# Kernel optimization log

Hardware: AMD Instinct MI355X
Metric: run time of the kernel (lower is better)

## Reference

```python
import jax, jax.numpy as jnp
import numpy as np

N = 50000      # nodes
E = 600000     # edges (before self-loops)
D_IN = 128     # input feature dim
HID = 128      # hidden_channels
HEADS1 = 8
OUT1 = HID // HEADS1  # 16 per head, concat -> 128
NEG_SLOPE = 0.2       # PyG GATConv default leaky_relu slope


def setup_inputs() -> dict:
    key = jax.random.key(0)
    ks = jax.random.split(key, 12)
    glorot = lambda k, shape: jax.random.normal(k, shape, jnp.float32) * np.sqrt(2.0 / (shape[0] + shape[-1]))
    x = jax.random.normal(ks[0], (N, D_IN), jnp.float32)
    edge_index = jax.random.randint(ks[1], (2, E), 0, N, dtype=jnp.int64)
    W1 = glorot(ks[2], (D_IN, HEADS1 * OUT1))
    att_src1 = glorot(ks[3], (HEADS1, OUT1))
    att_dst1 = glorot(ks[4], (HEADS1, OUT1))
    b1 = jnp.zeros((HEADS1 * OUT1,), jnp.float32)
    W2 = glorot(ks[5], (HID, HID))
    att_src2 = glorot(ks[6], (1, HID))
    att_dst2 = glorot(ks[7], (1, HID))
    b2 = jnp.zeros((HID,), jnp.float32)
    return {"x": x, "edge_index": edge_index,
            "W1": W1, "att_src1": att_src1, "att_dst1": att_dst1, "b1": b1,
            "W2": W2, "att_src2": att_src2, "att_dst2": att_dst2, "b2": b2}


def gat_conv(x, edge_index, W, a_src, a_dst, bias, concat):
    """PyG-style GATConv (eval mode: attention dropout disabled)."""
    n = x.shape[0]
    heads, out_ch = a_src.shape
    # add self-loops (PyG default add_self_loops=True)
    loop = jnp.arange(n, dtype=edge_index.dtype)
    src = jnp.concatenate([edge_index[0], loop])  # message source
    dst = jnp.concatenate([edge_index[1], loop])  # aggregation target
    h = (x @ W).reshape(n, heads, out_ch)                    # [n, H, C]
    alpha_src = jnp.sum(h * a_src[None], axis=-1)            # [n, H]
    alpha_dst = jnp.sum(h * a_dst[None], axis=-1)            # [n, H]
    e = alpha_src[src] + alpha_dst[dst]                      # [E+n, H]
    e = jnp.where(e > 0, e, NEG_SLOPE * e)                   # leaky_relu
    # segment softmax over incoming edges of each destination node
    e_max = jax.ops.segment_max(e, dst, num_segments=n)      # [n, H]
    ex = jnp.exp(e - e_max[dst])
    denom = jax.ops.segment_sum(ex, dst, num_segments=n)     # [n, H]
    alpha = ex / denom[dst]                                  # [E+n, H]
    msg = h[src] * alpha[:, :, None]                         # [E+n, H, C]
    out = jax.ops.segment_sum(msg, dst, num_segments=n)      # [n, H, C]
    out = out.reshape(n, heads * out_ch) if concat else out.mean(axis=1)
    return out + bias


def reference(x, edge_index, W1, att_src1, att_dst1, b1, W2, att_src2, att_dst2, b2):
    # eval mode: F.dropout is identity
    h = jax.nn.elu(gat_conv(x, edge_index, W1, att_src1, att_dst1, b1, concat=True))
    out = gat_conv(h, edge_index, W2, att_src2, att_dst2, b2, concat=False)
    return out
```

## Files before the change

### kernel.cpp

```cpp
#include <hip/hip_runtime.h>
#include <hip/hip_bf16.h>

#define NEG_SLOPE 0.2f

typedef short s16x8 __attribute__((ext_vector_type(8)));
typedef float f32x4 __attribute__((ext_vector_type(4)));

__device__ __forceinline__ unsigned short f2bf(float f) {
    unsigned int u = __float_as_uint(f);
    u += 0x7FFFu + ((u >> 16) & 1u);
    return (unsigned short)(u >> 16);
}


__global__ void zero_kernel(int* __restrict__ p, int count) {
    int i = blockIdx.x * blockDim.x + threadIdx.x;
    if (i < count) p[i] = 0;
}

__global__ __launch_bounds__(256) void hist_kernel(const int* __restrict__ ei, int e, int n,
                                                   int* __restrict__ ghist) {
    __shared__ int lh[256];
    int t = threadIdx.x;
    lh[t] = 0;
    __syncthreads();
    int base = blockIdx.x * 2048;
    int en = e + n;
#pragma unroll
    for (int q = 0; q < 8; ++q) {
        int i = base + q * 256 + t;
        if (i < en) {
            int dst = (i < e) ? ei[e + i] : (i - e);
            atomicAdd(&lh[dst >> 8], 1);
        }
    }
    __syncthreads();
    if (lh[t]) atomicAdd(&ghist[t], lh[t]);
}

__global__ __launch_bounds__(256) void bscan_kernel(const int* __restrict__ ghist,
                                                    int* __restrict__ gbase,
                                                    int* __restrict__ gcursor) {
    __shared__ int s[256];
    int t = threadIdx.x;
    int v = ghist[t];
    s[t] = v;
    __syncthreads();
    for (int off = 1; off < 256; off <<= 1) {
        int u = (t >= off) ? s[t - off] : 0;
        __syncthreads();
        s[t] += u;
        __syncthreads();
    }
    int ex = s[t] - v;
    gbase[t] = ex;
    gcursor[t] = ex;
}

__global__ __launch_bounds__(256) void scatter_kernel(const int* __restrict__ ei, int e, int n,
                                                      int* __restrict__ gcursor,
                                                      unsigned int* __restrict__ gpair) {
    __shared__ int lh[256], lbase[256];
    int t = threadIdx.x;
    lh[t] = 0;
    __syncthreads();
    int base = blockIdx.x * 2048;
    int en = e + n;
    int bk[8], rk[8];
    unsigned int pk[8];
#pragma unroll
    for (int q = 0; q < 8; ++q) {
        int i = base + q * 256 + t;
        bk[q] = -1;
        if (i < en) {
            int src, dst;
            if (i < e) { src = ei[i]; dst = ei[e + i]; }
            else       { src = i - e; dst = i - e; }
            int b = dst >> 8;
            bk[q] = b;
            rk[q] = atomicAdd(&lh[b], 1);
            pk[q] = (unsigned int)src | ((unsigned int)(dst & 255) << 16);
        }
    }
    __syncthreads();
    if (lh[t]) lbase[t] = atomicAdd(&gcursor[t], lh[t]);
    __syncthreads();
#pragma unroll
    for (int q = 0; q < 8; ++q)
        if (bk[q] >= 0) gpair[lbase[bk[q]] + rk[q]] = pk[q];
}

__global__ __launch_bounds__(256) void bucket_csr_kernel(const unsigned int* __restrict__ gpair,
                                                         const int* __restrict__ gbase,
                                                         int* __restrict__ rowptr,
                                                         int* __restrict__ colsrc, int n, int en) {
    int b = blockIdx.x, t = threadIdx.x;
    __shared__ int cnt[256], scn[256], cur[256];
    cnt[t] = 0;
    __syncthreads();
    int beg = gbase[b];
    int end = (b < 255) ? gbase[b + 1] : en;
    for (int i = beg + t; i < end; i += 256)
        atomicAdd(&cnt[gpair[i] >> 16], 1);
    __syncthreads();
    int v = cnt[t];
    scn[t] = v;
    __syncthreads();
    for (int off = 1; off < 256; off <<= 1) {
        int u = (t >= off) ? scn[t - off] : 0;
        __syncthreads();
        scn[t] += u;
        __syncthreads();
    }
    int ex = scn[t] - v;
    cur[t] = ex;
    int node = b * 256 + t;
    if (node < n) rowptr[node] = beg + ex;
    if (b == 0 && t == 0) rowptr[n] = en;
    __syncthreads();
    for (int i = beg + t; i < end; i += 256) {
        unsigned int p = gpair[i];
        int ofs = atomicAdd(&cur[p >> 16], 1);
        colsrc[beg + ofs] = (int)(p & 0xFFFFu);
    }
}


__global__ __launch_bounds__(256) void prep_w_kernel(const float* __restrict__ W1,
                                                     const float* __restrict__ as1,
                                                     const float* __restrict__ ad1,
                                                     unsigned short* __restrict__ Wf1,
                                                     const float* __restrict__ W2,
                                                     const float* __restrict__ as2,
                                                     const float* __restrict__ ad2,
                                                     unsigned short* __restrict__ Wf2) {
    int layer = blockIdx.x >> 2;
    int kt = blockIdx.x & 3;
    const float* W = layer ? W2 : W1;
    const float* as_v = layer ? as2 : as1;
    const float* ad_v = layer ? ad2 : ad1;
    unsigned short* Wf = layer ? Wf2 : Wf1;
    int H = layer ? 1 : 8;
    int t = threadIdx.x;
    for (int task = t; task < 9 * 64; task += 256) {
        int ct = task / 64, l = task & 63;
        int kbase = kt * 32 + (l >> 4) * 8;
        int c = l & 15;
        unsigned short o[8];
        if (ct < 8) {
            int col = ct * 16 + c;
#pragma unroll
            for (int j = 0; j < 8; ++j) o[j] = f2bf(W[(size_t)(kbase + j) * 128 + col]);
        } else {
#pragma unroll
            for (int j = 0; j < 8; ++j) {
                float s = 0.f;
                if (H == 8) {
                    const float* a = (c < 8) ? as_v : ad_v;
                    int hh = c & 7;
                    for (int m = 0; m < 16; ++m)
                        s += W[(size_t)(kbase + j) * 128 + hh * 16 + m] * a[hh * 16 + m];
                } else if (c < 2) {
                    const float* a = (c == 0) ? as_v : ad_v;
                    for (int m = 0; m < 128; ++m)
                        s += W[(size_t)(kbase + j) * 128 + m] * a[m];
                }
                o[j] = f2bf(s);
            }
        }
        *(uint4*)&Wf[(((size_t)kt * 9 + ct) * 64 + l) * 8] = *(uint4*)o;
    }
}


template <int H, bool INBF16>
__global__ __launch_bounds__(256) void gemm_mfma_kernel(const void* __restrict__ Xv,
                                                        const unsigned short* __restrict__ Wf,
                                                        unsigned short* __restrict__ Ob,
                                                        float* __restrict__ as_out,
                                                        float* __restrict__ ad_out, int n) {
    __shared__ unsigned short lds[26624];
    int tid = threadIdx.x;
    int row0 = blockIdx.x * 64;

    {
        const uint4* src = (const uint4*)Wf;
        uint4* dst = (uint4*)&lds[8192];
#pragma unroll
        for (int i = 0; i < 9; ++i) dst[tid + 256 * i] = src[tid + 256 * i];
    }
#pragma unroll
    for (int q = 0; q < 4; ++q) {
        int task = tid + q * 256;
        int r = task >> 4, kc = task & 15;
        int gr = row0 + r;
        uint4 val = make_uint4(0, 0, 0, 0);
        if (gr < n) {
            if (INBF16) {
                val = *(const uint4*)((const unsigned short*)Xv + (size_t)gr * 128 + kc * 8);
            } else {
                const float4* xp = (const float4*)((const float*)Xv + (size_t)gr * 128 + kc * 8);
                float4 x0 = xp[0], x1 = xp[1];
                unsigned short o[8] = {f2bf(x0.x), f2bf(x0.y), f2bf(x0.z), f2bf(x0.w),
                                       f2bf(x1.x), f2bf(x1.y), f2bf(x1.z), f2bf(x1.w)};
                val = *(uint4*)o;
            }
        }
        int w = r >> 4, kt = kc >> 2, lane = ((kc & 3) << 4) + (r & 15);
        *(uint4*)&lds[(size_t)(((w * 4 + kt) * 64) + lane) * 8] = val;
    }
    __syncthreads();

    int w = tid >> 6, l = tid & 63;
    f32x4 acc[9];
#pragma unroll
    for (int ct = 0; ct < 9; ++ct) acc[ct] = (f32x4){0.f, 0.f, 0.f, 0.f};
#pragma unroll
    for (int kt = 0; kt < 4; ++kt) {
        s16x8 a = *(s16x8*)&lds[(size_t)((w * 4 + kt) * 64 + l) * 8];
#pragma unroll
        for (int ct = 0; ct < 9; ++ct) {
            s16x8 b = *(s16x8*)&lds[8192 + (size_t)((kt * 9 + ct) * 64 + l) * 8];
            acc[ct] = __builtin_amdgcn_mfma_f32_16x16x32_bf16(a, b, acc[ct], 0, 0, 0);
        }
    }

    int c = l & 15, rgrp = l >> 4;
    int rowb = row0 + w * 16 + rgrp * 4;
#pragma unroll
    for (int reg = 0; reg < 4; ++reg) {
        int row = rowb + reg;
        if (row < n) {
#pragma unroll
            for (int ct = 0; ct < 8; ++ct)
                Ob[(size_t)row * 128 + ct * 16 + c] = f2bf(acc[ct][reg]);
            float av = acc[8][reg];
            if (H == 8) {
                if (c < 8) as_out[(size_t)row * 8 + c] = av;
                else       ad_out[(size_t)row * 8 + (c - 8)] = av;
            } else {
                if (c == 0)      as_out[row] = av;
                else if (c == 1) ad_out[row] = av;
            }
        }
    }
}


template <int H, int OBF>
__global__ __launch_bounds__(256) void agg_kernel(const int* __restrict__ rowptr,
                                                  const int* __restrict__ colsrc,
                                                  const unsigned short* __restrict__ hb,
                                                  const float* __restrict__ as,
                                                  const float* __restrict__ ad,
                                                  const float* __restrict__ bias,
                                                  void* __restrict__ outv, int n) {
    int tid = threadIdx.x;
    int node = blockIdx.x * 8 + (tid >> 5);
    int sub = tid & 31;
    int slot = sub >> 4;
    int cl = sub & 15;
    if (node >= n) return;
    int beg = rowptr[node];
    int end = rowptr[node + 1];
    int head = (H == 8) ? (cl >> 1) : 0;
    float adh = ad[(size_t)node * H + head];

    float acc[8];
#pragma unroll
    for (int c = 0; c < 8; ++c) acc[c] = 0.f;
    float den = 0.f;

#pragma unroll 2
    for (int i = beg + slot; i < end; i += 2) {
        int s = colsrc[i];
        float ev = as[(size_t)s * H + head] + adh;
        ev = (ev > 0.f) ? ev : NEG_SLOPE * ev;
        float wgt = __expf(ev);
        den += wgt;
        uint4 a = *(const uint4*)(hb + (size_t)s * 128 + cl * 8);
        unsigned int u[4] = {a.x, a.y, a.z, a.w};
#pragma unroll
        for (int k = 0; k < 4; ++k) {
            float lo = __uint_as_float(u[k] << 16);
            float hi = __uint_as_float(u[k] & 0xffff0000u);
            acc[2 * k]     += wgt * lo;
            acc[2 * k + 1] += wgt * hi;
        }
    }

    den += __shfl_xor(den, 16, 64);
#pragma unroll
    for (int c = 0; c < 8; ++c) acc[c] += __shfl_xor(acc[c], 16, 64);

    if (slot == 0) {
        float inv = 1.0f / den;
        float r[8];
#pragma unroll
        for (int k = 0; k < 8; ++k) {
            r[k] = acc[k] * inv + bias[cl * 8 + k];
            if (OBF) r[k] = (r[k] > 0.f) ? r[k] : expm1f(r[k]);
        }
        if (OBF) {
            unsigned short o[8];
#pragma unroll
            for (int k = 0; k < 8; ++k) o[k] = f2bf(r[k]);
            *(uint4*)((unsigned short*)outv + (size_t)node * 128 + cl * 8) = *(uint4*)o;
        } else {
            float4* p = (float4*)((float*)outv + (size_t)node * 128 + cl * 8);
            p[0] = make_float4(r[0], r[1], r[2], r[3]);
            p[1] = make_float4(r[4], r[5], r[6], r[7]);
        }
    }
}


extern "C" void kernel_launch(void* const* d_in, const int* in_sizes, int n_in,
                              void* d_out, int out_size, void* d_ws, size_t ws_size,
                              hipStream_t stream) {
    const float* x    = (const float*)d_in[0];
    const int*   ei   = (const int*)d_in[1];
    const float* W1   = (const float*)d_in[2];
    const float* a_s1 = (const float*)d_in[3];
    const float* a_d1 = (const float*)d_in[4];
    const float* b1   = (const float*)d_in[5];
    const float* W2   = (const float*)d_in[6];
    const float* a_s2 = (const float*)d_in[7];
    const float* a_d2 = (const float*)d_in[8];
    const float* b2   = (const float*)d_in[9];

    const int n  = in_sizes[0] / 128;
    const int e  = in_sizes[1] / 2;
    const int en = e + n;
    const int nbuck = (n + 255) >> 8;
    const int echunks = (en + 2047) / 2048;

    char* ws = (char*)d_ws;
    size_t off = 0;
    auto alloc = [&](size_t bytes) -> void* {
        void* p = ws + off;
        off += (bytes + 255) & ~(size_t)255;
        return p;
    };
    unsigned short* hb   = (unsigned short*)alloc((size_t)n * 128 * 2);
    unsigned short* hmid = (unsigned short*)alloc((size_t)n * 128 * 2);
    float* as1    = (float*)alloc((size_t)n * 8 * 4);
    float* ad1    = (float*)alloc((size_t)n * 8 * 4);
    float* as2    = (float*)alloc((size_t)n * 4);
    float* ad2    = (float*)alloc((size_t)n * 4);
    int*   rowptr = (int*)alloc((size_t)(n + 1) * 4);
    int*   colsrc = (int*)alloc((size_t)en * 4);
    unsigned int* gpair = (unsigned int*)alloc((size_t)en * 4);
    int*   ghist  = (int*)alloc(256 * 4);
    int*   gbase  = (int*)alloc(256 * 4);
    int*   gcursor= (int*)alloc(256 * 4);
    unsigned short* Wf1 = (unsigned short*)alloc(4 * 9 * 64 * 8 * 2);
    unsigned short* Wf2 = (unsigned short*)alloc(4 * 9 * 64 * 8 * 2);

    zero_kernel<<<1, 256, 0, stream>>>(ghist, 256);
    hist_kernel<<<echunks, 256, 0, stream>>>(ei, e, n, ghist);
    bscan_kernel<<<1, 256, 0, stream>>>(ghist, gbase, gcursor);
    scatter_kernel<<<echunks, 256, 0, stream>>>(ei, e, n, gcursor, gpair);
    bucket_csr_kernel<<<nbuck, 256, 0, stream>>>(gpair, gbase, rowptr, colsrc, n, en);

    prep_w_kernel<<<8, 256, 0, stream>>>(W1, a_s1, a_d1, Wf1, W2, a_s2, a_d2, Wf2);

    int gemm_grid = (n + 63) / 64;
    int node_grid = (n + 7) / 8;

    gemm_mfma_kernel<8, false><<<gemm_grid, 256, 0, stream>>>(x, Wf1, hb, as1, ad1, n);
    agg_kernel<8, 1><<<node_grid, 256, 0, stream>>>(rowptr, colsrc, hb, as1, ad1, b1, hmid, n);

    gemm_mfma_kernel<1, true><<<gemm_grid, 256, 0, stream>>>(hmid, Wf2, hb, as2, ad2, n);
    agg_kernel<1, 0><<<node_grid, 256, 0, stream>>>(rowptr, colsrc, hb, as2, ad2, b2, d_out, n);

    (void)n_in; (void)out_size; (void)ws_size;
}
```

Measured before the change: 149.4 us.

## Drop histogram pass with fixed-capacity buckets and read GEMM weights from global

After: 133.6 us. -10.5%, faster.

```diff
diff --git a/kernel.cpp b/kernel.cpp
--- a/kernel.cpp
+++ b/kernel.cpp
@@ -2,6 +2,7 @@
 #include <hip/hip_bf16.h>
 
 #define NEG_SLOPE 0.2f
+#define BCAP 8192
 
 typedef short s16x8 __attribute__((ext_vector_type(8)));
 typedef float f32x4 __attribute__((ext_vector_type(4)));
@@ -10,119 +11,6 @@
     unsigned int u = __float_as_uint(f);
     u += 0x7FFFu + ((u >> 16) & 1u);
     return (unsigned short)(u >> 16);
-}
-
-
-__global__ void zero_kernel(int* __restrict__ p, int count) {
-    int i = blockIdx.x * blockDim.x + threadIdx.x;
-    if (i < count) p[i] = 0;
-}
-
-__global__ __launch_bounds__(256) void hist_kernel(const int* __restrict__ ei, int e, int n,
-                                                   int* __restrict__ ghist) {
-    __shared__ int lh[256];
-    int t = threadIdx.x;
-    lh[t] = 0;
-    __syncthreads();
-    int base = blockIdx.x * 2048;
-    int en = e + n;
-#pragma unroll
-    for (int q = 0; q < 8; ++q) {
-        int i = base + q * 256 + t;
-        if (i < en) {
-            int dst = (i < e) ? ei[e + i] : (i - e);
-            atomicAdd(&lh[dst >> 8], 1);
-        }
-    }
-    __syncthreads();
-    if (lh[t]) atomicAdd(&ghist[t], lh[t]);
-}
-
-__global__ __launch_bounds__(256) void bscan_kernel(const int* __restrict__ ghist,
-                                                    int* __restrict__ gbase,
-                                                    int* __restrict__ gcursor) {
-    __shared__ int s[256];
-    int t = threadIdx.x;
-    int v = ghist[t];
-    s[t] = v;
-    __syncthreads();
-    for (int off = 1; off < 256; off <<= 1) {
-        int u = (t >= off) ? s[t - off] : 0;
-        __syncthreads();
-        s[t] += u;
-        __syncthreads();
-    }
-    int ex = s[t] - v;
-    gbase[t] = ex;
-    gcursor[t] = ex;
-}
-
-__global__ __launch_bounds__(256) void scatter_kernel(const int* __restrict__ ei, int e, int n,
-                                                      int* __restrict__ gcursor,
-                                                      unsigned int* __restrict__ gpair) {
-    __shared__ int lh[256], lbase[256];
-    int t = threadIdx.x;
-    lh[t] = 0;
-    __syncthreads();
-    int base = blockIdx.x * 2048;
-    int en = e + n;
-    int bk[8], rk[8];
-    unsigned int pk[8];
-#pragma unroll
-    for (int q = 0; q < 8; ++q) {
-        int i = base + q * 256 + t;
-        bk[q] = -1;
-        if (i < en) {
-            int src, dst;
-            if (i < e) { src = ei[i]; dst = ei[e + i]; }
-            else       { src = i - e; dst = i - e; }
-            int b = dst >> 8;
-            bk[q] = b;
-            rk[q] = atomicAdd(&lh[b], 1);
-            pk[q] = (unsigned int)src | ((unsigned int)(dst & 255) << 16);
-        }
-    }
-    __syncthreads();
-    if (lh[t]) lbase[t] = atomicAdd(&gcursor[t], lh[t]);
-    __syncthreads();
-#pragma unroll
-    for (int q = 0; q < 8; ++q)
-        if (bk[q] >= 0) gpair[lbase[bk[q]] + rk[q]] = pk[q];
-}
-
-__global__ __launch_bounds__(256) void bucket_csr_kernel(const unsigned int* __restrict__ gpair,
-                                                         const int* __restrict__ gbase,
-                                                         int* __restrict__ rowptr,
-                                                         int* __restrict__ colsrc, int n, int en) {
-    int b = blockIdx.x, t = threadIdx.x;
-    __shared__ int cnt[256], scn[256], cur[256];
-    cnt[t] = 0;
-    __syncthreads();
-    int beg = gbase[b];
-    int end = (b < 255) ? gbase[b + 1] : en;
-    for (int i = beg + t; i < end; i += 256)
-        atomicAdd(&cnt[gpair[i] >> 16], 1);
-    __syncthreads();
-    int v = cnt[t];
-    scn[t] = v;
-    __syncthreads();
-    for (int off = 1; off < 256; off <<= 1) {
-        int u = (t >= off) ? scn[t - off] : 0;
-        __syncthreads();
-        scn[t] += u;
-        __syncthreads();
-    }
-    int ex = scn[t] - v;
-    cur[t] = ex;
-    int node = b * 256 + t;
-    if (node < n) rowptr[node] = beg + ex;
-    if (b == 0 && t == 0) rowptr[n] = en;
-    __syncthreads();
-    for (int i = beg + t; i < end; i += 256) {
-        unsigned int p = gpair[i];
-        int ofs = atomicAdd(&cur[p >> 16], 1);
-        colsrc[beg + ofs] = (int)(p & 0xFFFFu);
-    }
 }
 
 
@@ -133,15 +21,23 @@
                                                      const float* __restrict__ W2,
                                                      const float* __restrict__ as2,
                                                      const float* __restrict__ ad2,
-                                                     unsigned short* __restrict__ Wf2) {
-    int layer = blockIdx.x >> 2;
-    int kt = blockIdx.x & 3;
+                                                     unsigned short* __restrict__ Wf2,
+                                                     int* __restrict__ gcursor,
+                                                     int* __restrict__ rowptr, int n, int en) {
+    int bid = blockIdx.x;
+    int t = threadIdx.x;
+    if (bid == 8) {
+        gcursor[t] = 0;
+        if (t == 0) rowptr[n] = en;
+        return;
+    }
+    int layer = bid >> 2;
+    int kt = bid & 3;
     const float* W = layer ? W2 : W1;
     const float* as_v = layer ? as2 : as1;
     const float* ad_v = layer ? ad2 : ad1;
     unsigned short* Wf = layer ? Wf2 : Wf1;
     int H = layer ? 1 : 8;
-    int t = threadIdx.x;
     for (int task = t; task < 9 * 64; task += 256) {
         int ct = task / 64, l = task & 63;
         int kbase = kt * 32 + (l >> 4) * 8;
@@ -173,22 +69,94 @@
 }
 
 
+__global__ __launch_bounds__(256) void scatter_kernel(const int* __restrict__ ei, int e, int n,
+                                                      int* __restrict__ gcursor,
+                                                      unsigned int* __restrict__ gpair) {
+    __shared__ int lh[256], lbase[256];
+    int t = threadIdx.x;
+    lh[t] = 0;
+    __syncthreads();
+    int base = blockIdx.x * 2048;
+    int en = e + n;
+    int bk[8], rk[8];
+    unsigned int pk[8];
+#pragma unroll
+    for (int q = 0; q < 8; ++q) {
+        int i = base + q * 256 + t;
+        bk[q] = -1;
+        if (i < en) {
+            int src, dst;
+            if (i < e) { src = ei[i]; dst = ei[e + i]; }
+            else       { src = i - e; dst = i - e; }
+            int b = dst >> 8;
+            bk[q] = b;
+            rk[q] = atomicAdd(&lh[b], 1);
+            pk[q] = (unsigned int)src | ((unsigned int)(dst & 255) << 16);
+        }
+    }
+    __syncthreads();
+    if (lh[t]) lbase[t] = atomicAdd(&gcursor[t], lh[t]);
+    __syncthreads();
+#pragma unroll
+    for (int q = 0; q < 8; ++q)
+        if (bk[q] >= 0) gpair[(size_t)bk[q] * BCAP + lbase[bk[q]] + rk[q]] = pk[q];
+}
+
+
+__global__ __launch_bounds__(256) void bucket_csr_kernel(const unsigned int* __restrict__ gpair,
+                                                         const int* __restrict__ gcursor,
+                                                         int* __restrict__ rowptr,
+                                                         int* __restrict__ colsrc, int n) {
+    int b = blockIdx.x, t = threadIdx.x;
+    __shared__ int bscan[256], cnt[256], scn[256], cur[256];
+    int bc = gcursor[t];
+    bscan[t] = bc;
+    cnt[t] = 0;
+    __syncthreads();
+    for (int off = 1; off < 256; off <<= 1) {
+        int u = (t >= off) ? bscan[t - off] : 0;
+        __syncthreads();
+        bscan[t] += u;
+        __syncthreads();
+    }
+    int mybase = bscan[b] - gcursor[b];
+    int mycnt = gcursor[b];
+    const unsigned int* mypair = gpair + (size_t)b * BCAP;
+    for (int i = t; i < mycnt; i += 256)
+        atomicAdd(&cnt[mypair[i] >> 16], 1);
+    __syncthreads();
+    int v = cnt[t];
+    scn[t] = v;
+    __syncthreads();
+    for (int off = 1; off < 256; off <<= 1) {
+        int u = (t >= off) ? scn[t - off] : 0;
+        __syncthreads();
+        scn[t] += u;
+        __syncthreads();
+    }
+    int ex = scn[t] - v;
+    cur[t] = ex;
+    int node = b * 256 + t;
+    if (node < n) rowptr[node] = mybase + ex;
+    __syncthreads();
+    for (int i = t; i < mycnt; i += 256) {
+        unsigned int p = mypair[i];
+        int ofs = atomicAdd(&cur[p >> 16], 1);
+        colsrc[mybase + ofs] = (int)(p & 0xFFFFu);
+    }
+}
+
+
 template <int H, bool INBF16>
 __global__ __launch_bounds__(256) void gemm_mfma_kernel(const void* __restrict__ Xv,
                                                         const unsigned short* __restrict__ Wf,
                                                         unsigned short* __restrict__ Ob,
                                                         float* __restrict__ as_out,
                                                         float* __restrict__ ad_out, int n) {
-    __shared__ unsigned short lds[26624];
+    __shared__ unsigned short lds[8192];
     int tid = threadIdx.x;
     int row0 = blockIdx.x * 64;
 
-    {
-        const uint4* src = (const uint4*)Wf;
-        uint4* dst = (uint4*)&lds[8192];
-#pragma unroll
-        for (int i = 0; i < 9; ++i) dst[tid + 256 * i] = src[tid + 256 * i];
-    }
 #pragma unroll
     for (int q = 0; q < 4; ++q) {
         int task = tid + q * 256;
@@ -212,16 +180,21 @@
     __syncthreads();
 
     int w = tid >> 6, l = tid & 63;
+    s16x8 a[4];
+#pragma unroll
+    for (int kt = 0; kt < 4; ++kt)
+        a[kt] = *(s16x8*)&lds[(size_t)((w * 4 + kt) * 64 + l) * 8];
+
+    const s16x8* bp = (const s16x8*)Wf;
     f32x4 acc[9];
 #pragma unroll
     for (int ct = 0; ct < 9; ++ct) acc[ct] = (f32x4){0.f, 0.f, 0.f, 0.f};
 #pragma unroll
-    for (int kt = 0; kt < 4; ++kt) {
-        s16x8 a = *(s16x8*)&lds[(size_t)((w * 4 + kt) * 64 + l) * 8];
-#pragma unroll
-        for (int ct = 0; ct < 9; ++ct) {
-            s16x8 b = *(s16x8*)&lds[8192 + (size_t)((kt * 9 + ct) * 64 + l) * 8];
-            acc[ct] = __builtin_amdgcn_mfma_f32_16x16x32_bf16(a, b, acc[ct], 0, 0, 0);
+    for (int ct = 0; ct < 9; ++ct) {
+#pragma unroll
+        for (int kt = 0; kt < 4; ++kt) {
+            s16x8 b = bp[(kt * 9 + ct) * 64 + l];
+            acc[ct] = __builtin_amdgcn_mfma_f32_16x16x32_bf16(a[kt], b, acc[ct], 0, 0, 0);
         }
     }
 
@@ -350,20 +323,15 @@
     float* ad2    = (float*)alloc((size_t)n * 4);
     int*   rowptr = (int*)alloc((size_t)(n + 1) * 4);
     int*   colsrc = (int*)alloc((size_t)en * 4);
-    unsigned int* gpair = (unsigned int*)alloc((size_t)en * 4);
-    int*   ghist  = (int*)alloc(256 * 4);
-    int*   gbase  = (int*)alloc(256 * 4);
+    unsigned int* gpair = (unsigned int*)alloc((size_t)nbuck * BCAP * 4);
     int*   gcursor= (int*)alloc(256 * 4);
     unsigned short* Wf1 = (unsigned short*)alloc(4 * 9 * 64 * 8 * 2);
     unsigned short* Wf2 = (unsigned short*)alloc(4 * 9 * 64 * 8 * 2);
 
-    zero_kernel<<<1, 256, 0, stream>>>(ghist, 256);
-    hist_kernel<<<echunks, 256, 0, stream>>>(ei, e, n, ghist);
-    bscan_kernel<<<1, 256, 0, stream>>>(ghist, gbase, gcursor);
+    prep_w_kernel<<<9, 256, 0, stream>>>(W1, a_s1, a_d1, Wf1, W2, a_s2, a_d2, Wf2,
+                                         gcursor, rowptr, n, en);
     scatter_kernel<<<echunks, 256, 0, stream>>>(ei, e, n, gcursor, gpair);
-    bucket_csr_kernel<<<nbuck, 256, 0, stream>>>(gpair, gbase, rowptr, colsrc, n, en);
-
-    prep_w_kernel<<<8, 256, 0, stream>>>(W1, a_s1, a_d1, Wf1, W2, a_s2, a_d2, Wf2);
+    bucket_csr_kernel<<<nbuck, 256, 0, stream>>>(gpair, gcursor, rowptr, colsrc, n);
 
     int gemm_grid = (n + 63) / 64;
     int node_grid = (n + 7) / 8;
```
